# Optimization experiments

Hardware: AMD Instinct MI355X
Metric: run time of the kernel (lower is better)

The kernel has to match this reference:

```python
import jax, jax.numpy as jnp
import numpy as np

D_MODEL = 512

def setup_inputs() -> dict:
    key = jax.random.key(0)
    k1, k2, k3, k4, k5 = jax.random.split(key, 5)
    x = jax.random.normal(k1, (8, D_MODEL, 2048), dtype=jnp.float32)
    s = 1.0 / np.sqrt(D_MODEL)
    W_qkv = jax.random.uniform(k2, (D_MODEL, 3 * D_MODEL), dtype=jnp.float32, minval=-s, maxval=s)
    b_qkv = jax.random.uniform(k3, (3 * D_MODEL,), dtype=jnp.float32, minval=-s, maxval=s)
    W_proj = jax.random.uniform(k4, (D_MODEL, D_MODEL), dtype=jnp.float32, minval=-s, maxval=s)
    b_proj = jax.random.uniform(k5, (D_MODEL,), dtype=jnp.float32, minval=-s, maxval=s)
    return {"x": x, "W_qkv": W_qkv, "b_qkv": b_qkv, "W_proj": W_proj, "b_proj": b_proj}

def reference(x, W_qkv, b_qkv, W_proj, b_proj):
    # x: [B, L, N] with L == d_model; attend across the N variable axis
    xt = jnp.swapaxes(x, 1, 2)                      # [B, N, L]
    L = xt.shape[-1]
    qkv = xt @ W_qkv + b_qkv                        # [B, N, 3L]
    q, k, v = jnp.split(qkv, 3, axis=-1)            # each [B, N, L]
    attn = jnp.einsum('bnd,bmd->bnm', q, k) / jnp.sqrt(jnp.float32(L))
    attn = jax.nn.softmax(attn, axis=-1)            # [B, N, N]
    out = jnp.einsum('bnm,bmd->bnd', attn, v)       # [B, N, L]
    out = out @ W_proj + b_proj                     # [B, N, L]
    return jnp.swapaxes(out, 1, 2)                  # [B, L, N]
```

## Files before the change

kernel.cpp:

```cpp
#include <hip/hip_runtime.h>

#define NVAR 2048
#define DM   512
#define J3   1536

typedef _Float16 f16;
typedef _Float16 f16x8 __attribute__((ext_vector_type(8)));
typedef _Float16 f16x4 __attribute__((ext_vector_type(4)));
typedef float    f32x4 __attribute__((ext_vector_type(4)));

#define GLOAD(gp, lp) __builtin_amdgcn_global_load_lds( \
    (const __attribute__((address_space(1))) void*)(gp), \
    (__attribute__((address_space(3))) void*)(lp), 16, 0, 0)

__global__ __launch_bounds__(256)
void k_tr(const float* __restrict__ src, f16* __restrict__ dst,
          int R, int C, long bsSrc, long bsDst) {
    __shared__ float t[64][65];
    const float* s = src + (size_t)blockIdx.z * bsSrc;
    f16* d = dst + (size_t)blockIdx.z * bsDst;
    const int c0 = blockIdx.x * 64, r0 = blockIdx.y * 64;
    const int lx = threadIdx.x & 15, ly = threadIdx.x >> 4;
#pragma unroll
    for (int p = 0; p < 4; ++p) {
        int r = p * 16 + ly;
        f32x4 v = *(const f32x4*)(s + (size_t)(r0 + r) * C + c0 + lx * 4);
#pragma unroll
        for (int i = 0; i < 4; ++i) t[r][lx * 4 + i] = v[i];
    }
    __syncthreads();
#pragma unroll
    for (int p = 0; p < 4; ++p) {
        int c = p * 16 + ly;
        f16x4 h;
#pragma unroll
        for (int i = 0; i < 4; ++i) h[i] = (f16)t[lx * 4 + i][c];
        *(f16x4*)(d + (size_t)(c0 + c) * R + r0 + lx * 4) = h;
    }
}

__global__ __launch_bounds__(512, 2)
void gemm_big(const f16* __restrict__ A, const f16* __restrict__ B,
              long bsA, long bsB, int lda, int ldb, int K, int nbx,
              float scale, f16* __restrict__ o0) {
    __shared__ f16 sA[256 * 64];
    __shared__ f16 sB[256 * 64];
    const int tid  = threadIdx.x;
    const int lane = tid & 63;
    const int w    = __builtin_amdgcn_readfirstlane(tid >> 6);
    const int wm   = (w >> 2) * 128;
    const int wn   = (w & 3) * 64;
    const int z    = blockIdx.x;
    const int bid  = blockIdx.y;
    const int bxA  = bid % nbx;
    const int bxB  = bid / nbx;

    const f16* Ab = A + (size_t)z * bsA + (size_t)bxA * 256 * lda;
    const f16* Bb = B + (size_t)z * bsB + (size_t)bxB * 256 * ldb;

    int srcA[4], srcB[4];
#pragma unroll
    for (int i = 0; i < 4; ++i) {
        int slot = i * 512 + tid;
        int row  = slot >> 3;
        int s    = (slot & 7) ^ (row & 7);
        srcA[i] = row * lda + s * 8;
        srcB[i] = row * ldb + s * 8;
    }

    int koff[2];
#pragma unroll
    for (int ks = 0; ks < 2; ++ks)
        koff[ks] = ((ks * 4 + (lane >> 4)) ^ (lane & 7)) * 8;
    const int rowA = (wm + (lane & 15)) * 64;
    const int rowB = (wn + (lane & 15)) * 64;

    f32x4 acc[8][4] = {};

    for (int k0 = 0; k0 < K; k0 += 64) {
        __syncthreads();
#pragma unroll
        for (int i = 0; i < 4; ++i)
            GLOAD(Ab + srcA[i] + k0, sA + i * 4096 + w * 512);
#pragma unroll
        for (int i = 0; i < 4; ++i)
            GLOAD(Bb + srcB[i] + k0, sB + i * 4096 + w * 512);
        __syncthreads();

        f16x8 bv[4][2];
#pragma unroll
        for (int nj = 0; nj < 4; ++nj)
#pragma unroll
            for (int ks = 0; ks < 2; ++ks)
                bv[nj][ks] = *(const f16x8*)(sB + rowB + nj * 1024 + koff[ks]);
#pragma unroll
        for (int h = 0; h < 2; ++h) {
            f16x8 av[4][2];
#pragma unroll
            for (int mi = 0; mi < 4; ++mi)
#pragma unroll
                for (int ks = 0; ks < 2; ++ks)
                    av[mi][ks] = *(const f16x8*)(sA + rowA + (h * 4 + mi) * 1024 + koff[ks]);
#pragma unroll
            for (int mi = 0; mi < 4; ++mi)
#pragma unroll
                for (int nj = 0; nj < 4; ++nj)
#pragma unroll
                    for (int ks = 0; ks < 2; ++ks)
                        acc[h * 4 + mi][nj] = __builtin_amdgcn_mfma_f32_16x16x32_f16(
                            av[mi][ks], bv[nj][ks], acc[h * 4 + mi][nj], 0, 0, 0);
        }
    }

    const int rb0 = bxA * 256 + wm + (lane >> 4) * 4;
    const int cb0 = bxB * 256 + wn + (lane & 15);
#pragma unroll
    for (int mi = 0; mi < 8; ++mi)
#pragma unroll
        for (int nj = 0; nj < 4; ++nj) {
            f16x4 vv;
#pragma unroll
            for (int r = 0; r < 4; ++r)
                vv[r] = (f16)__expf(acc[mi][nj][r] * scale);
            *(f16x4*)(o0 + ((size_t)z * NVAR + cb0 + nj * 16) * NVAR
                           + rb0 + mi * 16) = vv;
        }
}

template<int MODE>
__global__ __launch_bounds__(256)
void gemm_f16(const f16* __restrict__ A, const f16* __restrict__ B,
              long bsA, long bsB, int lda, int ldb, int K, int nbx,
              const float* __restrict__ bias,
              f16* __restrict__ o0, f16* __restrict__ o1, f16* __restrict__ o2,
              float* __restrict__ of) {
    __shared__ f16 sA[128 * 64];
    __shared__ f16 sB[128 * 64];
    const int tid  = threadIdx.x;
    const int lane = tid & 63;
    const int w    = __builtin_amdgcn_readfirstlane(tid >> 6);
    const int wm   = (w >> 1) * 64;
    const int wn   = (w & 1) * 64;
    const int z    = blockIdx.x;
    const int bid  = blockIdx.y;
    const int bxA  = bid % nbx;
    const int bxB  = bid / nbx;

    const f16* Ab = A + (size_t)z * bsA + (size_t)bxA * 128 * lda;
    const f16* Bb = B + (size_t)z * bsB + (size_t)bxB * 128 * ldb;

    int srcA[4], srcB[4];
#pragma unroll
    for (int i = 0; i < 4; ++i) {
        int slot = i * 256 + tid;
        int row  = slot >> 3;
        int s    = (slot & 7) ^ (row & 7);
        srcA[i] = row * lda + s * 8;
        srcB[i] = row * ldb + s * 8;
    }

    f16x8 ones;
#pragma unroll
    for (int e = 0; e < 8; ++e) ones[e] = (f16)1.0f;

    f32x4 acc[4][4] = {};
    f32x4 accrs[4] = {};

    for (int k0 = 0; k0 < K; k0 += 64) {
        __syncthreads();
#pragma unroll
        for (int i = 0; i < 4; ++i) {
            GLOAD(Ab + srcA[i] + k0, sA + i * 2048 + w * 512);
            GLOAD(Bb + srcB[i] + k0, sB + i * 2048 + w * 512);
        }
        __syncthreads();
#pragma unroll
        for (int kh = 0; kh < 2; ++kh) {
            f16x8 av[4], bv[4];
#pragma unroll
            for (int mi = 0; mi < 4; ++mi) {
                int r = wm + mi * 16 + (lane & 15);
                int s = (kh * 4 + (lane >> 4)) ^ (r & 7);
                av[mi] = *(const f16x8*)(sA + r * 64 + s * 8);
            }
#pragma unroll
            for (int nj = 0; nj < 4; ++nj) {
                int r = wn + nj * 16 + (lane & 15);
                int s = (kh * 4 + (lane >> 4)) ^ (r & 7);
                bv[nj] = *(const f16x8*)(sB + r * 64 + s * 8);
            }
            if constexpr (MODE == 2) {
#pragma unroll
                for (int nj = 0; nj < 4; ++nj)
                    accrs[nj] = __builtin_amdgcn_mfma_f32_16x16x32_f16(
                        ones, bv[nj], accrs[nj], 0, 0, 0);
            }
#pragma unroll
            for (int mi = 0; mi < 4; ++mi)
#pragma unroll
                for (int nj = 0; nj < 4; ++nj)
                    acc[mi][nj] = __builtin_amdgcn_mfma_f32_16x16x32_f16(
                        av[mi], bv[nj], acc[mi][nj], 0, 0, 0);
        }
    }

    const int rb0 = bxA * 128 + wm + (lane >> 4) * 4;
    const int cb0 = bxB * 128 + wn + (lane & 15);

    if (MODE == 0) {
        const int seg = (bxA * 128) >> 9;
#pragma unroll
        for (int mi = 0; mi < 4; ++mi) {
            const int j = rb0 + mi * 16;
            const f32x4 b4 = *(const f32x4*)(bias + j);
#pragma unroll
            for (int nj = 0; nj < 4; ++nj) {
                const int n = cb0 + nj * 16;
                if (seg == 2) {
#pragma unroll
                    for (int r = 0; r < 4; ++r)
                        o2[((size_t)z * DM + (j - 1024 + r)) * NVAR + n] =
                            (f16)(acc[mi][nj][r] + b4[r]);
                } else {
                    f16* dst = seg ? o1 : o0;
                    const int jj = seg ? j - 512 : j;
                    f16x4 vv;
#pragma unroll
                    for (int r = 0; r < 4; ++r) vv[r] = (f16)(acc[mi][nj][r] + b4[r]);
                    *(f16x4*)(dst + ((size_t)z * NVAR + n) * DM + jj) = vv;
                }
            }
        }
    } else if (MODE == 2) {
        float inv[4];
#pragma unroll
        for (int nj = 0; nj < 4; ++nj) inv[nj] = 1.0f / accrs[nj][0];
#pragma unroll
        for (int mi = 0; mi < 4; ++mi)
#pragma unroll
            for (int nj = 0; nj < 4; ++nj) {
                f16x4 vv;
#pragma unroll
                for (int r = 0; r < 4; ++r)
                    vv[r] = (f16)(acc[mi][nj][r] * inv[nj]);
                *(f16x4*)(o0 + ((size_t)z * NVAR + cb0 + nj * 16) * DM
                               + rb0 + mi * 16) = vv;
            }
    } else {
#pragma unroll
        for (int mi = 0; mi < 4; ++mi)
#pragma unroll
            for (int nj = 0; nj < 4; ++nj) {
                const int l = cb0 + nj * 16;
                const float bb = bias[l];
                f32x4 vv;
#pragma unroll
                for (int r = 0; r < 4; ++r) vv[r] = acc[mi][nj][r] + bb;
                *(f32x4*)(of + ((size_t)z * DM + l) * NVAR + rb0 + mi * 16) = vv;
            }
    }
}

extern "C" void kernel_launch(void* const* d_in, const int* in_sizes, int n_in,
                              void* d_out, int out_size, void* d_ws, size_t ws_size,
                              hipStream_t stream) {
    const float* x     = (const float*)d_in[0];
    const float* Wqkv  = (const float*)d_in[1];
    const float* bqkv  = (const float*)d_in[2];
    const float* Wproj = (const float*)d_in[3];
    const float* bproj = (const float*)d_in[4];
    float* out = (float*)d_out;

    const size_t PB = (size_t)NVAR * DM;
    f16* xT  = (f16*)d_ws;
    f16* q   = xT + 8 * PB;
    f16* kk  = q  + 8 * PB;
    f16* vT  = kk + 8 * PB;
    f16* S   = vT + 8 * PB;
    f16* O   = S  + (size_t)8 * NVAR * NVAR;
    f16* WqT = O  + 8 * PB;
    f16* WpT = WqT + (size_t)J3 * DM;

    k_tr<<<dim3(NVAR / 64, DM / 64, 8), 256, 0, stream>>>(
        x, xT, DM, NVAR, (long)DM * NVAR, (long)NVAR * DM);
    k_tr<<<dim3(J3 / 64, DM / 64, 1), 256, 0, stream>>>(Wqkv, WqT, DM, J3, 0, 0);
    k_tr<<<dim3(DM / 64, DM / 64, 1), 256, 0, stream>>>(Wproj, WpT, DM, DM, 0, 0);

    gemm_f16<0><<<dim3(8, 12 * 16), 256, 0, stream>>>(
        WqT, xT, 0, (long)NVAR * DM, DM, DM, DM, 12,
        bqkv, q, kk, vT, nullptr);

    gemm_big<<<dim3(8, 8 * 8), 512, 0, stream>>>(
        kk, q, (long)NVAR * DM, (long)NVAR * DM, DM, DM, DM, 8,
        0.044194173824159216f, S);

    gemm_f16<2><<<dim3(8, 4 * 16), 256, 0, stream>>>(
        vT, S, (long)DM * NVAR, (long)NVAR * NVAR, NVAR, NVAR, NVAR, 4,
        nullptr, O, nullptr, nullptr, nullptr);

    gemm_f16<3><<<dim3(8, 16 * 4), 256, 0, stream>>>(
        O, WpT, (long)NVAR * DM, 0, DM, DM, DM, 16,
        bproj, nullptr, nullptr, nullptr, out);
}
```

Baseline: 184.1 us.

## Software-pipeline score GEMM with multi-buffered LDS and split MFMA phases

```diff
diff --git a/kernel.cpp b/kernel.cpp
--- a/kernel.cpp
+++ b/kernel.cpp
@@ -9,9 +9,29 @@
 typedef _Float16 f16x4 __attribute__((ext_vector_type(4)));
 typedef float    f32x4 __attribute__((ext_vector_type(4)));
 
+#define SBAR() do { asm volatile("s_barrier" ::: "memory"); \
+                    __builtin_amdgcn_sched_barrier(0); } while(0)
+#define LGKM0() do { asm volatile("s_waitcnt lgkmcnt(0)" ::: "memory"); \
+                     __builtin_amdgcn_sched_barrier(0); } while(0)
 #define GLOAD(gp, lp) __builtin_amdgcn_global_load_lds( \
     (const __attribute__((address_space(1))) void*)(gp), \
     (__attribute__((address_space(3))) void*)(lp), 16, 0, 0)
+
+__device__ __forceinline__ void waitvm_n(int n) {
+    switch (n) {
+    case 0: asm volatile("s_waitcnt vmcnt(0)" ::: "memory"); break;
+    case 1: asm volatile("s_waitcnt vmcnt(1)" ::: "memory"); break;
+    case 2: asm volatile("s_waitcnt vmcnt(2)" ::: "memory"); break;
+    case 3: asm volatile("s_waitcnt vmcnt(3)" ::: "memory"); break;
+    case 4: asm volatile("s_waitcnt vmcnt(4)" ::: "memory"); break;
+    case 5: asm volatile("s_waitcnt vmcnt(5)" ::: "memory"); break;
+    case 6: asm volatile("s_waitcnt vmcnt(6)" ::: "memory"); break;
+    case 7: asm volatile("s_waitcnt vmcnt(7)" ::: "memory"); break;
+    case 8: asm volatile("s_waitcnt vmcnt(8)" ::: "memory"); break;
+    default: break;
+    }
+    __builtin_amdgcn_sched_barrier(0);
+}
 
 __global__ __launch_bounds__(256)
 void k_tr(const float* __restrict__ src, f16* __restrict__ dst,
@@ -39,12 +59,15 @@
     }
 }
 
+#define ASZ (256 * 64)
 __global__ __launch_bounds__(512, 2)
-void gemm_big(const f16* __restrict__ A, const f16* __restrict__ B,
-              long bsA, long bsB, int lda, int ldb, int K, int nbx,
-              float scale, f16* __restrict__ o0) {
-    __shared__ f16 sA[256 * 64];
-    __shared__ f16 sB[256 * 64];
+void gemm_sp(const f16* __restrict__ A, const f16* __restrict__ B,
+             long bsA, long bsB, int lda, int ldb, int K,
+             float scale, f16* __restrict__ o0) {
+    __shared__ f16 smem[5 * ASZ];
+    f16* sA = smem;
+    f16* sB = smem + 3 * ASZ;
+
     const int tid  = threadIdx.x;
     const int lane = tid & 63;
     const int w    = __builtin_amdgcn_readfirstlane(tid >> 6);
@@ -52,21 +75,36 @@
     const int wn   = (w & 3) * 64;
     const int z    = blockIdx.x;
     const int bid  = blockIdx.y;
-    const int bxA  = bid % nbx;
-    const int bxB  = bid / nbx;
+    const int bxA  = bid & 7;
+    const int bxB  = bid >> 3;
 
     const f16* Ab = A + (size_t)z * bsA + (size_t)bxA * 256 * lda;
     const f16* Bb = B + (size_t)z * bsB + (size_t)bxB * 256 * ldb;
 
-    int srcA[4], srcB[4];
-#pragma unroll
-    for (int i = 0; i < 4; ++i) {
-        int slot = i * 512 + tid;
-        int row  = slot >> 3;
-        int s    = (slot & 7) ^ (row & 7);
-        srcA[i] = row * lda + s * 8;
-        srcB[i] = row * ldb + s * 8;
-    }
+    int offA[2][2], offB[2][2];
+#pragma unroll
+    for (int h = 0; h < 2; ++h)
+#pragma unroll
+        for (int i = 0; i < 2; ++i) {
+            int slot = i * 512 + tid;
+            int row  = h * 128 + (slot >> 3);
+            int s    = (slot & 7) ^ (row & 7);
+            offA[h][i] = row * lda + s * 8;
+            offB[h][i] = row * ldb + s * 8;
+        }
+
+    auto STG_A = [&](int kt, int h, int buf) {
+        f16* d = sA + buf * ASZ + h * 8192;
+#pragma unroll
+        for (int i = 0; i < 2; ++i)
+            GLOAD(Ab + offA[h][i] + kt * 64, d + (i * 512 + tid) * 8);
+    };
+    auto STG_B = [&](int kt, int h, int buf) {
+        f16* d = sB + buf * ASZ + h * 8192;
+#pragma unroll
+        for (int i = 0; i < 2; ++i)
+            GLOAD(Bb + offB[h][i] + kt * 64, d + (i * 512 + tid) * 8);
+    };
 
     int koff[2];
 #pragma unroll
@@ -75,41 +113,74 @@
     const int rowA = (wm + (lane & 15)) * 64;
     const int rowB = (wn + (lane & 15)) * 64;
 
+    f16x8 av[8][2], bv[4][2];
     f32x4 acc[8][4] = {};
 
-    for (int k0 = 0; k0 < K; k0 += 64) {
-        __syncthreads();
-#pragma unroll
-        for (int i = 0; i < 4; ++i)
-            GLOAD(Ab + srcA[i] + k0, sA + i * 4096 + w * 512);
-#pragma unroll
-        for (int i = 0; i < 4; ++i)
-            GLOAD(Bb + srcB[i] + k0, sB + i * 4096 + w * 512);
-        __syncthreads();
-
-        f16x8 bv[4][2];
-#pragma unroll
-        for (int nj = 0; nj < 4; ++nj)
+    auto LD_AV = [&](const f16* p, int mi0) {
+#pragma unroll
+        for (int mi = 0; mi < 4; ++mi)
 #pragma unroll
             for (int ks = 0; ks < 2; ++ks)
-                bv[nj][ks] = *(const f16x8*)(sB + rowB + nj * 1024 + koff[ks]);
-#pragma unroll
-        for (int h = 0; h < 2; ++h) {
-            f16x8 av[4][2];
-#pragma unroll
-            for (int mi = 0; mi < 4; ++mi)
+                av[mi0 + mi][ks] = *(const f16x8*)(p + rowA + (mi0 + mi) * 1024 + koff[ks]);
+    };
+    auto LD_BV = [&](const f16* p, int nj0) {
+#pragma unroll
+        for (int nj = 0; nj < 2; ++nj)
+#pragma unroll
+            for (int ks = 0; ks < 2; ++ks)
+                bv[nj0 + nj][ks] = *(const f16x8*)(p + rowB + (nj0 + nj) * 1024 + koff[ks]);
+    };
+    auto MM = [&](int mi0, int nj0) {
+        __builtin_amdgcn_s_setprio(1);
+#pragma unroll
+        for (int mi = 0; mi < 4; ++mi)
+#pragma unroll
+            for (int nj = 0; nj < 2; ++nj)
 #pragma unroll
                 for (int ks = 0; ks < 2; ++ks)
-                    av[mi][ks] = *(const f16x8*)(sA + rowA + (h * 4 + mi) * 1024 + koff[ks]);
-#pragma unroll
-            for (int mi = 0; mi < 4; ++mi)
-#pragma unroll
-                for (int nj = 0; nj < 4; ++nj)
-#pragma unroll
-                    for (int ks = 0; ks < 2; ++ks)
-                        acc[h * 4 + mi][nj] = __builtin_amdgcn_mfma_f32_16x16x32_f16(
-                            av[mi][ks], bv[nj][ks], acc[h * 4 + mi][nj], 0, 0, 0);
-        }
+                    acc[mi0 + mi][nj0 + nj] = __builtin_amdgcn_mfma_f32_16x16x32_f16(
+                        av[mi0 + mi][ks], bv[nj0 + nj][ks], acc[mi0 + mi][nj0 + nj], 0, 0, 0);
+        __builtin_amdgcn_s_setprio(0);
+    };
+
+    const int NT = K >> 6;
+    int issued = 0, markB = 0;
+
+    STG_A(0, 0, 0); STG_A(0, 1, 0); issued += 4;
+    STG_B(0, 0, 0); STG_B(0, 1, 0); issued += 4; markB = issued;
+    if (NT > 1) { STG_A(1, 0, 1); STG_A(1, 1, 1); issued += 4; }
+    waitvm_n(issued - markB);
+    SBAR();
+
+    int iA = 0, iB = 0;
+    for (int t = 0; t < NT; ++t) {
+        const f16* pA = sA + iA * ASZ;
+        const f16* pB = sB + iB * ASZ;
+        const int bufB2 = iB ^ 1;
+        int bufA2 = iA + 2; if (bufA2 >= 3) bufA2 -= 3;
+
+        LD_BV(pB, 0); LD_AV(pA, 0);
+        if (t + 1 < NT) { STG_B(t + 1, 0, bufB2); issued += 2; }
+        SBAR(); LGKM0();
+        MM(0, 0);
+        SBAR();
+        LD_BV(pB, 2);
+        if (t + 1 < NT) { STG_B(t + 1, 1, bufB2); issued += 2; markB = issued; }
+        SBAR(); LGKM0();
+        MM(0, 2);
+        SBAR();
+        LD_AV(pA, 4);
+        if (t + 2 < NT) { STG_A(t + 2, 0, bufA2); issued += 2; }
+        SBAR(); LGKM0();
+        MM(4, 2);
+        SBAR();
+        if (t + 2 < NT) { STG_A(t + 2, 1, bufA2); issued += 2; }
+        if (t + 1 < NT) { waitvm_n(issued - markB); SBAR(); }
+        MM(4, 0);
+        if (t + 1 < NT) SBAR();
+
+        iA = (iA + 1 == 3) ? 0 : iA + 1;
+        iB ^= 1;
     }
 
     const int rb0 = bxA * 256 + wm + (lane >> 4) * 4;
@@ -290,8 +361,8 @@
         WqT, xT, 0, (long)NVAR * DM, DM, DM, DM, 12,
         bqkv, q, kk, vT, nullptr);
 
-    gemm_big<<<dim3(8, 8 * 8), 512, 0, stream>>>(
-        kk, q, (long)NVAR * DM, (long)NVAR * DM, DM, DM, DM, 8,
+    gemm_sp<<<dim3(8, 8 * 8), 512, 0, stream>>>(
+        kk, q, (long)NVAR * DM, (long)NVAR * DM, DM, DM, DM,
         0.044194173824159216f, S);
 
     gemm_f16<2><<<dim3(8, 4 * 16), 256, 0, stream>>>(
```

Measured after the change: 180.4 us. -2.0%, faster.
